# Optimization experiments

Measured on AMD Instinct MI355X. Metric: run time of the kernel, lower is better.

## Reference

```python
import jax, jax.numpy as jnp
import numpy as np

SEQ, BATCH, HID, LAYERS = 512, 64, 1024, 2

def setup_inputs() -> dict:
    key = jax.random.key(0)
    ks = jax.random.split(key, 5)
    scale = 1.0 / np.sqrt(2 * HID)
    return {
        "input": jax.random.normal(ks[0], (SEQ, BATCH, HID), dtype=jnp.float32),
        "h0": jax.random.normal(ks[1], (LAYERS, BATCH, HID), dtype=jnp.float32),
        "c0": jax.random.normal(ks[2], (LAYERS, BATCH, HID), dtype=jnp.float32),
        "W": jax.random.normal(ks[3], (LAYERS, 2 * HID, 4 * HID), dtype=jnp.float32) * scale,
        "b": jax.random.normal(ks[4], (LAYERS, 4 * HID), dtype=jnp.float32) * scale,
    }

def reference(input, h0, c0, W, b):
    num_layers = W.shape[0]

    def step(carry, x_t):
        h, c = carry  # each [L, B, H]
        hs, cs = [], []
        layer_in = x_t  # [B, H]
        for l in range(num_layers):
            concat_in = jnp.concatenate([layer_in, h[l]], axis=1)  # [B, 2H]
            gates = concat_in @ W[l] + b[l]                        # [B, 4H]
            i, j, f, o = jnp.split(gates, 4, axis=1)
            c_new = c[l] * jax.nn.sigmoid(f) + jax.nn.sigmoid(i) * jnp.tanh(j)
            h_new = jnp.tanh(c_new) * jax.nn.sigmoid(o)
            hs.append(h_new)
            cs.append(c_new)
            layer_in = h_new
        return (jnp.stack(hs), jnp.stack(cs)), layer_in

    (last_hidden, last_cell), final_output = jax.lax.scan(step, (h0, c0), input)
    return final_output, (last_hidden, last_cell)
```

## Files before the change

kernel.cpp:

```cpp
#include <hip/hip_runtime.h>


typedef _Float16 half8 __attribute__((ext_vector_type(8)));
typedef float    f32x4 __attribute__((ext_vector_type(4)));
typedef unsigned long long u64;
typedef unsigned int u32;

#define SEQ 512
#define BATCH 64
#define HID 1024
#define NBLK 128
#define SLSZ 65536

__device__ int g_sync[1024];

__global__ void init_bar_k() {
    for (int i = threadIdx.x; i < 1024; i += 256) g_sync[i] = 0;
}

__global__ void zero_out(float* __restrict__ out) {
    size_t i = (size_t)blockIdx.x * blockDim.x + threadIdx.x;
    ((f32x4*)out)[i] = f32x4{0.f, 0.f, 0.f, 0.f};
}

__global__ void pack1(const float* __restrict__ src, _Float16* __restrict__ dst) {
    int nt   = blockIdx.x;
    int ktg  = blockIdx.y;
    int lane = threadIdx.x & 63;
    int wave = threadIdx.x >> 6;
    int kt   = ktg * 4 + wave;
    int k0 = kt * 32 + (lane >> 4) * 8;
    int n  = nt * 16 + (lane & 15);
    half8 v;
#pragma unroll
    for (int j = 0; j < 8; ++j)
        v[j] = (_Float16)src[(size_t)(k0 + j) * 4096 + n];
    *(half8*)(dst + ((size_t)(nt * 32 + kt) * 64 + lane) * 8) = v;
}

__global__ void pack_wh(const float* __restrict__ src, _Float16* __restrict__ dst) {
    int g    = blockIdx.x;
    int ktg  = blockIdx.y;
    int lane = threadIdx.x & 63;
    int wave = threadIdx.x >> 6;
    int kt   = ktg * 4 + wave;
    int c16  = lane & 15;
    int k0   = kt * 32 + (lane >> 4) * 8;
#pragma unroll
    for (int tau = 0; tau < 2; ++tau) {
        int col = (tau * 2 + (c16 >> 3)) * 1024 + g * 8 + (c16 & 7);
        half8 v;
#pragma unroll
        for (int j = 0; j < 8; ++j)
            v[j] = (_Float16)src[(size_t)(k0 + j) * 4096 + col];
        *(half8*)(dst + ((size_t)((g * 2 + tau) * 32 + kt) * 64 + lane) * 8) = v;
    }
}

__global__ void copy_f4(const float* __restrict__ src, float* __restrict__ dst) {
    int i = blockIdx.x * blockDim.x + threadIdx.x;
    ((f32x4*)dst)[i] = ((const f32x4*)src)[i];
}

__global__ __launch_bounds__(256) void gemm_in(
    const float* __restrict__ A, const _Float16* __restrict__ Bp,
    const float* __restrict__ bias, _Float16* __restrict__ Gout)
{
    int lane = threadIdx.x & 63;
    int wave = threadIdx.x >> 6;
    int wm = wave & 1, wn = wave >> 1;
    int m0 = blockIdx.x * 128 + wm * 64;
    int n0 = blockIdx.y * 128 + wn * 64;
    int col = lane & 15, quad = lane >> 4;
    f32x4 acc[4][4] = {};
    const float*    Arow  = A + (size_t)(m0 + col) * 1024 + quad * 8;
    const _Float16* Bbase = Bp + (size_t)(n0 >> 4) * 16384 + (size_t)lane * 8;
    for (int kt = 0; kt < 32; ++kt) {
        half8 a[4], b[4];
#pragma unroll
        for (int i = 0; i < 4; ++i) {
            const float* p = Arow + (size_t)i * 16 * 1024 + kt * 32;
            f32x4 v0 = *(const f32x4*)(p);
            f32x4 v1 = *(const f32x4*)(p + 4);
            a[i][0] = (_Float16)v0[0]; a[i][1] = (_Float16)v0[1];
            a[i][2] = (_Float16)v0[2]; a[i][3] = (_Float16)v0[3];
            a[i][4] = (_Float16)v1[0]; a[i][5] = (_Float16)v1[1];
            a[i][6] = (_Float16)v1[2]; a[i][7] = (_Float16)v1[3];
        }
#pragma unroll
        for (int j = 0; j < 4; ++j)
            b[j] = *(const half8*)(Bbase + (size_t)j * 16384 + kt * 512);
#pragma unroll
        for (int i = 0; i < 4; ++i)
#pragma unroll
            for (int j = 0; j < 4; ++j)
                acc[i][j] = __builtin_amdgcn_mfma_f32_16x16x32_f16(a[i], b[j], acc[i][j], 0, 0, 0);
    }
#pragma unroll
    for (int j = 0; j < 4; ++j) {
        int n = n0 + j * 16 + col;
        float bv = bias[n];
#pragma unroll
        for (int i = 0; i < 4; ++i)
#pragma unroll
            for (int r = 0; r < 4; ++r) {
                int m = m0 + i * 16 + quad * 4 + r;
                Gout[(size_t)m * 4096 + n] = (_Float16)(acc[i][j][r] + bv);
            }
    }
}

__device__ __forceinline__ void grid_barrier(int n) {
    __syncthreads();
    if (threadIdx.x == 0) {
        const int grp = (int)(blockIdx.x & 7);
        int v = __hip_atomic_fetch_add(&g_sync[grp * 64], 1,
                                       __ATOMIC_RELAXED, __HIP_MEMORY_SCOPE_AGENT);
        if (v == n * 16 - 1) {
            int gv = __hip_atomic_fetch_add(&g_sync[576], 1,
                                            __ATOMIC_RELAXED, __HIP_MEMORY_SCOPE_AGENT);
            if (gv == n * 8 - 1)
                __hip_atomic_store(&g_sync[704], n,
                                   __ATOMIC_RELAXED, __HIP_MEMORY_SCOPE_AGENT);
        }
        while (__hip_atomic_load(&g_sync[704],
                                 __ATOMIC_RELAXED, __HIP_MEMORY_SCOPE_AGENT) < n)
            __builtin_amdgcn_s_sleep(1);
    }
    __syncthreads();
}

__device__ __forceinline__ half8 cload8(const _Float16* p) {
    union { half8 h; u64 u[2]; } x;
    x.u[0] = __hip_atomic_load((const u64*)p, __ATOMIC_RELAXED, __HIP_MEMORY_SCOPE_AGENT);
    x.u[1] = __hip_atomic_load((const u64*)p + 1, __ATOMIC_RELAXED, __HIP_MEMORY_SCOPE_AGENT);
    return x.h;
}

__device__ __forceinline__ half8 cvt_row(const float* p) {
    f32x4 v0 = *(const f32x4*)p, v1 = *(const f32x4*)(p + 4);
    half8 a;
    a[0] = (_Float16)v0[0]; a[1] = (_Float16)v0[1];
    a[2] = (_Float16)v0[2]; a[3] = (_Float16)v0[3];
    a[4] = (_Float16)v1[0]; a[5] = (_Float16)v1[1];
    a[6] = (_Float16)v1[2]; a[7] = (_Float16)v1[3];
    return a;
}

template <bool F32, bool DO0, bool DO1>
__device__ __forceinline__ void passA(
    f32x4 (&acc0)[4][2], f32x4 (&acc1)[4][2], const void* src,
    const half8 (&b0)[2][8], const half8 (&b1)[2][8],
    int wave, int c16, int quad)
{
#pragma unroll
    for (int i = 0; i < 8; ++i) {
        const int k0 = (wave * 8 + i) * 32 + quad * 8;
        half8 a[4];
#pragma unroll
        for (int m = 0; m < 4; ++m) {
            if constexpr (F32)
                a[m] = cvt_row((const float*)src + (size_t)(m * 16 + c16) * HID + k0);
            else
                a[m] = cload8((const _Float16*)src + (size_t)(m * 16 + c16) * HID + k0);
        }
#pragma unroll
        for (int m = 0; m < 4; ++m) {
            if constexpr (DO0) {
                acc0[m][0] = __builtin_amdgcn_mfma_f32_16x16x32_f16(a[m], b0[0][i], acc0[m][0], 0, 0, 0);
                acc0[m][1] = __builtin_amdgcn_mfma_f32_16x16x32_f16(a[m], b0[1][i], acc0[m][1], 0, 0, 0);
            }
            if constexpr (DO1) {
                acc1[m][0] = __builtin_amdgcn_mfma_f32_16x16x32_f16(a[m], b1[0][i], acc1[m][0], 0, 0, 0);
                acc1[m][1] = __builtin_amdgcn_mfma_f32_16x16x32_f16(a[m], b1[1][i], acc1[m][1], 0, 0, 0);
            }
        }
    }
}

template <bool F32>
__device__ __forceinline__ void passB(
    f32x4 (&acc1)[4][2], const void* src, const half8* smw,
    int wave, int c16, int quad, int lane)
{
#pragma unroll
    for (int i = 0; i < 8; ++i) {
        const int k0 = (wave * 8 + i) * 32 + quad * 8;
        half8 a[4];
#pragma unroll
        for (int m = 0; m < 4; ++m) {
            if constexpr (F32)
                a[m] = cvt_row((const float*)src + (size_t)(m * 16 + c16) * HID + k0);
            else
                a[m] = cload8((const _Float16*)src + (size_t)(m * 16 + c16) * HID + k0);
        }
        half8 bw0 = smw[(size_t)((0 * 32 + wave * 8 + i) * 64 + lane)];
        half8 bw1 = smw[(size_t)((1 * 32 + wave * 8 + i) * 64 + lane)];
#pragma unroll
        for (int m = 0; m < 4; ++m) {
            acc1[m][0] = __builtin_amdgcn_mfma_f32_16x16x32_f16(a[m], bw0, acc1[m][0], 0, 0, 0);
            acc1[m][1] = __builtin_amdgcn_mfma_f32_16x16x32_f16(a[m], bw1, acc1[m][1], 0, 0, 0);
        }
    }
}

__device__ __forceinline__ void cell_epilogue(
    const f32x4 (&fin)[2], float (&creg)[4], _Float16* rw, float* outp,
    float* lh, float* lc, int rbase, int hcol, int c16, bool owner)
{
#pragma unroll
    for (int r = 0; r < 4; ++r) {
        float v0 = fin[0][r], v1 = fin[1][r];
        float x0 = __shfl_xor(v0, 8), x1 = __shfl_xor(v1, 8);
        float gi = owner ? v0 : x0, gj = owner ? x0 : v0;
        float gf = owner ? v1 : x1, go = owner ? x1 : v1;
        float iv = 1.f / (1.f + __expf(-gi));
        float jv = tanhf(gj);
        float fv = 1.f / (1.f + __expf(-gf));
        float ov = 1.f / (1.f + __expf(-go));
        float cn = creg[r] * fv + iv * jv;
        float hn = tanhf(cn) * ov;
        creg[r] = cn;
        union { _Float16 f; unsigned short s; } cv; cv.f = (_Float16)hn;
        u32 other = (u32)(unsigned short)__shfl_xor((int)cv.s, 1);
        size_t idx = (size_t)(rbase + r) * HID + hcol;
        if (owner) {
            if (outp) outp[idx] = hn;
            if (lh) { lh[idx] = hn; lc[idx] = cn; }
            if (!(c16 & 1)) {
                u32 pk = (u32)cv.s | (other << 16);
                __hip_atomic_store((u32*)(rw + idx), pk,
                                   __ATOMIC_RELAXED, __HIP_MEMORY_SCOPE_AGENT);
            }
        }
    }
}

__global__ __launch_bounds__(256, 1) void lstm_fused(
    const _Float16* __restrict__ WhR0, const _Float16* __restrict__ WxR1,
    const _Float16* __restrict__ WhR1, const _Float16* __restrict__ Gc,
    const float* __restrict__ hinit, _Float16* __restrict__ ring,
    float* __restrict__ cb, float* __restrict__ out,
    const float* __restrict__ bias1, int t0, int nsteps, int nbar0)
{
    const int lane = threadIdx.x & 63;
    const int wave = threadIdx.x >> 6;
    const int g = blockIdx.x;
    const int c16 = lane & 15, quad = lane >> 4;
    const int hcol = g * 8 + (c16 & 7);
    const bool owner = (c16 < 8);
    const int rbase = wave * 16 + quad * 4;

    __shared__ half8 smw[4096];
    __shared__ f32x4 red0[3][4][2][64];
    __shared__ f32x4 red1[3][4][2][64];

    _Float16* ring0 = ring;
    _Float16* ring1 = ring + 2 * SLSZ;
    const size_t FO = (size_t)SEQ * SLSZ;

    {
        const _Float16* wsrc = WhR1 + (size_t)g * 32768;
        for (int i = threadIdx.x; i < 4096; i += 256)
            smw[i] = *(const half8*)(wsrc + (size_t)i * 8);
    }

    half8 bh0[2][8], bx1[2][8];
#pragma unroll
    for (int tau = 0; tau < 2; ++tau)
#pragma unroll
        for (int i = 0; i < 8; ++i) {
            size_t off = ((size_t)((g * 2 + tau) * 32 + wave * 8 + i) * 64 + lane) * 8;
            bh0[tau][i] = *(const half8*)(WhR0 + off);
            bx1[tau][i] = *(const half8*)(WxR1 + off);
        }

    float bv1[2];
#pragma unroll
    for (int tau = 0; tau < 2; ++tau)
        bv1[tau] = bias1[(tau * 2 + (c16 >> 3)) * 1024 + hcol];

    float creg0[4], creg1[4];
#pragma unroll
    for (int r = 0; r < 4; ++r) {
        creg0[r] = cb[(size_t)(rbase + r) * HID + hcol];
        creg1[r] = cb[SLSZ + (size_t)(rbase + r) * HID + hcol];
    }

    const int colG0 = (c16 >> 3) * 1024 + hcol;
    __syncthreads();

    for (int tl = 0; tl < nsteps; ++tl) {
        const int s  = t0 + tl;
        const int t1 = s - 1;
        const bool do0 = (s < SEQ);
        const bool do1 = (t1 >= 0);

        f32x4 acc0[4][2], acc1[4][2];
#pragma unroll
        for (int m = 0; m < 4; ++m)
#pragma unroll
            for (int tau = 0; tau < 2; ++tau) {
                acc0[m][tau] = f32x4{0.f, 0.f, 0.f, 0.f};
                acc1[m][tau] = f32x4{0.f, 0.f, 0.f, 0.f};
            }
#pragma unroll
        for (int m = 0; m < 4; ++m)
            if (m == wave) {
                acc1[m][0] = f32x4{bv1[0], bv1[0], bv1[0], bv1[0]};
                acc1[m][1] = f32x4{bv1[1], bv1[1], bv1[1], bv1[1]};
            }
        if (do0) {
            const _Float16* Gt = Gc + (size_t)tl * 4 * SLSZ;
#pragma unroll
            for (int tau = 0; tau < 2; ++tau) {
                f32x4 v;
#pragma unroll
                for (int r = 0; r < 4; ++r)
                    v[r] = (float)Gt[(size_t)(rbase + r) * 4096 + tau * 2048 + colG0];
#pragma unroll
                for (int m = 0; m < 4; ++m)
                    if (m == wave) acc0[m][tau] = v;
            }
        }

        if (tl > 0) grid_barrier(nbar0 + tl);

        const _Float16* h0prev = ring0 + (size_t)((s - 1) & 1) * SLSZ;
        if (do0 && do1)
            passA<false, true, true>(acc0, acc1, h0prev, bh0, bx1, wave, c16, quad);
        else if (do0)
            passA<true, true, false>(acc0, acc1, hinit, bh0, bx1, wave, c16, quad);
        else
            passA<false, false, true>(acc0, acc1, h0prev, bh0, bx1, wave, c16, quad);

        if (do1) {
            if (t1 == 0)
                passB<true>(acc1, hinit + SLSZ, smw, wave, c16, quad, lane);
            else
                passB<false>(acc1, ring1 + (size_t)((t1 - 1) & 1) * SLSZ, smw,
                             wave, c16, quad, lane);
        }

        if (do0) {
#pragma unroll
            for (int m = 0; m < 4; ++m)
                if (m != wave) {
                    int slot = wave - (wave > m ? 1 : 0);
#pragma unroll
                    for (int tau = 0; tau < 2; ++tau)
                        red0[slot][m][tau][lane] = acc0[m][tau];
                }
        }
        if (do1) {
#pragma unroll
            for (int m = 0; m < 4; ++m)
                if (m != wave) {
                    int slot = wave - (wave > m ? 1 : 0);
#pragma unroll
                    for (int tau = 0; tau < 2; ++tau)
                        red1[slot][m][tau][lane] = acc1[m][tau];
                }
        }
        f32x4 own0[2], own1[2];
        own0[0] = acc0[0][0]; own0[1] = acc0[0][1];
        own1[0] = acc1[0][0]; own1[1] = acc1[0][1];
#pragma unroll
        for (int m = 1; m < 4; ++m)
            if (wave == m) {
                own0[0] = acc0[m][0]; own0[1] = acc0[m][1];
                own1[0] = acc1[m][0]; own1[1] = acc1[m][1];
            }
        __syncthreads();

        if (do0) {
            f32x4 fin[2];
#pragma unroll
            for (int tau = 0; tau < 2; ++tau) {
                f32x4 ssum = own0[tau];
#pragma unroll
                for (int v = 0; v < 3; ++v) ssum += red0[v][wave][tau][lane];
                fin[tau] = ssum;
            }
            float* lh = (s == SEQ - 1) ? out + FO : nullptr;
            float* lc = (s == SEQ - 1) ? out + FO + 2 * SLSZ : nullptr;
            cell_epilogue(fin, creg0, ring0 + (size_t)(s & 1) * SLSZ,
                          nullptr, lh, lc, rbase, hcol, c16, owner);
        }
        if (do1) {
            f32x4 fin[2];
#pragma unroll
            for (int tau = 0; tau < 2; ++tau) {
                f32x4 ssum = own1[tau];
#pragma unroll
                for (int v = 0; v < 3; ++v) ssum += red1[v][wave][tau][lane];
                fin[tau] = ssum;
            }
            float* lh = (t1 == SEQ - 1) ? out + FO + SLSZ : nullptr;
            float* lc = (t1 == SEQ - 1) ? out + FO + 3 * SLSZ : nullptr;
            cell_epilogue(fin, creg1, ring1 + (size_t)(t1 & 1) * SLSZ,
                          out + (size_t)t1 * SLSZ, lh, lc, rbase, hcol, c16, owner);
        }
    }

    if (owner) {
#pragma unroll
        for (int r = 0; r < 4; ++r) {
            cb[(size_t)(rbase + r) * HID + hcol] = creg0[r];
            cb[SLSZ + (size_t)(rbase + r) * HID + hcol] = creg1[r];
        }
    }
}

extern "C" void kernel_launch(void* const* d_in, const int* in_sizes, int n_in,
                              void* d_out, int out_size, void* d_ws, size_t ws_size,
                              hipStream_t stream) {
    const float* X  = (const float*)d_in[0];
    const float* h0 = (const float*)d_in[1];
    const float* c0 = (const float*)d_in[2];
    const float* W  = (const float*)d_in[3];
    const float* bb = (const float*)d_in[4];
    float* out = (float*)d_out;
    char* ws = (char*)d_ws;

    const size_t FIXED = 34603008ULL;
    int CH = 0;
    const int tiers[4] = {32, 16, 8, 4};
    for (int i = 0; i < 4; ++i)
        if (ws_size >= FIXED + (size_t)tiers[i] * 524288ULL) { CH = tiers[i]; break; }
    if (CH == 0) {
        zero_out<<<dim3(33024), 256, 0, stream>>>(out);
        return;
    }

    _Float16* WpX  = (_Float16*)(ws + 0);
    _Float16* WhR0 = (_Float16*)(ws + 8388608);
    _Float16* WxR1 = (_Float16*)(ws + 16777216);
    _Float16* WhR1 = (_Float16*)(ws + 25165824);
    _Float16* ring = (_Float16*)(ws + 33554432);
    float*    cb   = (float*)(ws + 34078720);
    _Float16* Gc   = (_Float16*)(ws + 34603008);

    const size_t MSTRIDE = 2048ULL * 4096ULL;
    const int MC = CH * BATCH;
    const int NCHUNK = SEQ / CH;

    pack1<<<dim3(256, 8), 256, 0, stream>>>(W, WpX);
    pack_wh<<<dim3(NBLK, 8), 256, 0, stream>>>(W + 1024 * 4096, WhR0);
    pack_wh<<<dim3(NBLK, 8), 256, 0, stream>>>(W + MSTRIDE, WxR1);
    pack_wh<<<dim3(NBLK, 8), 256, 0, stream>>>(W + MSTRIDE + 1024 * 4096, WhR1);
    copy_f4<<<dim3(128), 256, 0, stream>>>(c0, cb);
    init_bar_k<<<dim3(1), 256, 0, stream>>>();

    int nbar = 0;
    for (int chunk = 0; chunk < NCHUNK; ++chunk) {
        gemm_in<<<dim3(MC / 128, 32), 256, 0, stream>>>(
            X + (size_t)chunk * MC * 1024, WpX, bb, Gc);
        int nsteps = CH + (chunk == NCHUNK - 1 ? 1 : 0);
        lstm_fused<<<dim3(NBLK), 256, 0, stream>>>(
            WhR0, WxR1, WhR1, Gc, h0, ring, cb, out, bb + 4096,
            chunk * CH, nsteps, nbar);
        nbar += nsteps - 1;
    }
}
```

Before: 12.82 ms.

## Fuse input GEMM and recurrence into one persistent producer/consumer kernel

Replaces the per-chunk sequence of gemm_in plus lstm_fused launches with a single persistent kernel. 64 producer blocks compute the layer-0 input projection into a double-buffered chunk slot while 128 consumer blocks run the recurrent steps, with atomic flags handling the handoff. This removes per-chunk launch overhead and the serialization between GEMM and recurrence, and the cell state stays in registers across all steps instead of round-tripping through a workspace buffer. The grid barrier now spins on per-group release flags and drains outstanding memory ops before arriving. The risks are producer/consumer stalls, smaller chunks (8 or 4), and reliance on all 192 blocks being co-resident.

```diff
diff --git a/kernel.cpp b/kernel.cpp
--- a/kernel.cpp
+++ b/kernel.cpp
@@ -9,13 +9,14 @@
 #define SEQ 512
 #define BATCH 64
 #define HID 1024
-#define NBLK 128
+#define NCONS 128
+#define NPROD 64
 #define SLSZ 65536
 
-__device__ int g_sync[1024];
+__device__ int g_sync[8192];
 
 __global__ void init_bar_k() {
-    for (int i = threadIdx.x; i < 1024; i += 256) g_sync[i] = 0;
+    for (int i = threadIdx.x; i < 8192; i += 256) g_sync[i] = 0;
 }
 
 __global__ void zero_out(float* __restrict__ out) {
@@ -57,20 +58,16 @@
     }
 }
 
-__global__ void copy_f4(const float* __restrict__ src, float* __restrict__ dst) {
-    int i = blockIdx.x * blockDim.x + threadIdx.x;
-    ((f32x4*)dst)[i] = ((const f32x4*)src)[i];
-}
-
-__global__ __launch_bounds__(256) void gemm_in(
+__device__ __forceinline__ void gemm_tile(
     const float* __restrict__ A, const _Float16* __restrict__ Bp,
-    const float* __restrict__ bias, _Float16* __restrict__ Gout)
+    const float* __restrict__ bias, _Float16* __restrict__ Gout,
+    int mi, int ni)
 {
     int lane = threadIdx.x & 63;
     int wave = threadIdx.x >> 6;
     int wm = wave & 1, wn = wave >> 1;
-    int m0 = blockIdx.x * 128 + wm * 64;
-    int n0 = blockIdx.y * 128 + wn * 64;
+    int m0 = mi * 128 + wm * 64;
+    int n0 = ni * 128 + wn * 64;
     int col = lane & 15, quad = lane >> 4;
     f32x4 acc[4][4] = {};
     const float*    Arow  = A + (size_t)(m0 + col) * 1024 + quad * 8;
@@ -110,20 +107,23 @@
     }
 }
 
-__device__ __forceinline__ void grid_barrier(int n) {
+__device__ __forceinline__ void grid_barrier(int n, int grp) {
+    asm volatile("s_waitcnt vmcnt(0)" ::: "memory");
     __syncthreads();
     if (threadIdx.x == 0) {
-        const int grp = (int)(blockIdx.x & 7);
         int v = __hip_atomic_fetch_add(&g_sync[grp * 64], 1,
                                        __ATOMIC_RELAXED, __HIP_MEMORY_SCOPE_AGENT);
-        if (v == n * 16 - 1) {
-            int gv = __hip_atomic_fetch_add(&g_sync[576], 1,
+        if (v == n * (NCONS / 8) - 1) {
+            int gv = __hip_atomic_fetch_add(&g_sync[512], 1,
                                             __ATOMIC_RELAXED, __HIP_MEMORY_SCOPE_AGENT);
-            if (gv == n * 8 - 1)
-                __hip_atomic_store(&g_sync[704], n,
-                                   __ATOMIC_RELAXED, __HIP_MEMORY_SCOPE_AGENT);
-        }
-        while (__hip_atomic_load(&g_sync[704],
+            if (gv == n * 8 - 1) {
+#pragma unroll
+                for (int i = 0; i < 8; ++i)
+                    __hip_atomic_store(&g_sync[576 + i * 64], n,
+                                       __ATOMIC_RELAXED, __HIP_MEMORY_SCOPE_AGENT);
+            }
+        }
+        while (__hip_atomic_load(&g_sync[576 + grp * 64],
                                  __ATOMIC_RELAXED, __HIP_MEMORY_SCOPE_AGENT) < n)
             __builtin_amdgcn_s_sleep(1);
     }
@@ -236,20 +236,55 @@
     }
 }
 
-__global__ __launch_bounds__(256, 1) void lstm_fused(
-    const _Float16* __restrict__ WhR0, const _Float16* __restrict__ WxR1,
+__device__ __forceinline__ void producer_path(
+    const _Float16* __restrict__ WpX, const float* __restrict__ X,
+    const float* __restrict__ bias0, _Float16* __restrict__ Gc,
+    int nchunk, int ch)
+{
+    const int p = blockIdx.x;
+    const int rows = ch * 64;
+    const int tpp = (rows / 128) * 32 / NPROD;
+    const size_t slotsz = (size_t)ch * 4 * SLSZ;
+    for (int c = 0; c < nchunk; ++c) {
+        if (c >= 2) {
+            if (threadIdx.x == 0)
+                while (__hip_atomic_load(&g_sync[3136 + (c - 2) * 16],
+                                         __ATOMIC_RELAXED, __HIP_MEMORY_SCOPE_AGENT) < NCONS)
+                    __builtin_amdgcn_s_sleep(4);
+            __syncthreads();
+        }
+        const float* A = X + (size_t)c * rows * 1024;
+        _Float16* Gout = Gc + (size_t)(c & 1) * slotsz;
+        for (int tt = 0; tt < tpp; ++tt) {
+            int T = p * tpp + tt;
+            gemm_tile(A, WpX, bias0, Gout, T >> 5, T & 31);
+        }
+        asm volatile("s_waitcnt vmcnt(0)" ::: "memory");
+        __syncthreads();
+        if (threadIdx.x == 0) {
+            __builtin_amdgcn_fence(__ATOMIC_RELEASE, "agent");
+            __hip_atomic_fetch_add(&g_sync[1088 + c * 16], 1,
+                                   __ATOMIC_RELAXED, __HIP_MEMORY_SCOPE_AGENT);
+        }
+        __syncthreads();
+    }
+}
+
+__device__ __forceinline__ void consumer_path(
+    int g, const _Float16* __restrict__ WhR0, const _Float16* __restrict__ WxR1,
     const _Float16* __restrict__ WhR1, const _Float16* __restrict__ Gc,
-    const float* __restrict__ hinit, _Float16* __restrict__ ring,
-    float* __restrict__ cb, float* __restrict__ out,
-    const float* __restrict__ bias1, int t0, int nsteps, int nbar0)
+    const float* __restrict__ hinit, const float* __restrict__ cinit,
+    _Float16* __restrict__ ring, float* __restrict__ out,
+    const float* __restrict__ bias1, int ch)
 {
     const int lane = threadIdx.x & 63;
     const int wave = threadIdx.x >> 6;
-    const int g = blockIdx.x;
     const int c16 = lane & 15, quad = lane >> 4;
     const int hcol = g * 8 + (c16 & 7);
     const bool owner = (c16 < 8);
     const int rbase = wave * 16 + quad * 4;
+    const int grp = g & 7;
+    const size_t slotsz = (size_t)ch * 4 * SLSZ;
 
     __shared__ half8 smw[4096];
     __shared__ f32x4 red0[3][4][2][64];
@@ -264,7 +299,6 @@
         for (int i = threadIdx.x; i < 4096; i += 256)
             smw[i] = *(const half8*)(wsrc + (size_t)i * 8);
     }
-
     half8 bh0[2][8], bx1[2][8];
 #pragma unroll
     for (int tau = 0; tau < 2; ++tau)
@@ -274,7 +308,6 @@
             bh0[tau][i] = *(const half8*)(WhR0 + off);
             bx1[tau][i] = *(const half8*)(WxR1 + off);
         }
-
     float bv1[2];
 #pragma unroll
     for (int tau = 0; tau < 2; ++tau)
@@ -283,18 +316,28 @@
     float creg0[4], creg1[4];
 #pragma unroll
     for (int r = 0; r < 4; ++r) {
-        creg0[r] = cb[(size_t)(rbase + r) * HID + hcol];
-        creg1[r] = cb[SLSZ + (size_t)(rbase + r) * HID + hcol];
+        creg0[r] = cinit[(size_t)(rbase + r) * HID + hcol];
+        creg1[r] = cinit[SLSZ + (size_t)(rbase + r) * HID + hcol];
     }
 
     const int colG0 = (c16 >> 3) * 1024 + hcol;
     __syncthreads();
 
-    for (int tl = 0; tl < nsteps; ++tl) {
-        const int s  = t0 + tl;
-        const int t1 = s - 1;
-        const bool do0 = (s < SEQ);
-        const bool do1 = (t1 >= 0);
+    for (int sidx = 0; sidx <= SEQ; ++sidx) {
+        const int s = sidx, t1 = s - 1;
+        const bool do0 = (s < SEQ), do1 = (t1 >= 0);
+        int cchunk = 0, tl = 0;
+        if (do0) { cchunk = s / ch; tl = s - cchunk * ch; }
+
+        if (do0 && tl == 0) {
+            if (threadIdx.x == 0) {
+                while (__hip_atomic_load(&g_sync[1088 + cchunk * 16],
+                                         __ATOMIC_RELAXED, __HIP_MEMORY_SCOPE_AGENT) < NPROD)
+                    __builtin_amdgcn_s_sleep(1);
+                __builtin_amdgcn_fence(__ATOMIC_ACQUIRE, "agent");
+            }
+            __syncthreads();
+        }
 
         f32x4 acc0[4][2], acc1[4][2];
 #pragma unroll
@@ -311,7 +354,7 @@
                 acc1[m][1] = f32x4{bv1[1], bv1[1], bv1[1], bv1[1]};
             }
         if (do0) {
-            const _Float16* Gt = Gc + (size_t)tl * 4 * SLSZ;
+            const _Float16* Gt = Gc + (size_t)(cchunk & 1) * slotsz + (size_t)tl * 4 * SLSZ;
 #pragma unroll
             for (int tau = 0; tau < 2; ++tau) {
                 f32x4 v;
@@ -324,7 +367,10 @@
             }
         }
 
-        if (tl > 0) grid_barrier(nbar0 + tl);
+        if (sidx > 0) grid_barrier(sidx, grp);
+        if (do0 && tl == ch - 1 && threadIdx.x == 0)
+            __hip_atomic_fetch_add(&g_sync[3136 + cchunk * 16], 1,
+                                   __ATOMIC_RELAXED, __HIP_MEMORY_SCOPE_AGENT);
 
         const _Float16* h0prev = ring0 + (size_t)((s - 1) & 1) * SLSZ;
         if (do0 && do1)
@@ -402,14 +448,23 @@
                           out + (size_t)t1 * SLSZ, lh, lc, rbase, hcol, c16, owner);
         }
     }
-
-    if (owner) {
-#pragma unroll
-        for (int r = 0; r < 4; ++r) {
-            cb[(size_t)(rbase + r) * HID + hcol] = creg0[r];
-            cb[SLSZ + (size_t)(rbase + r) * HID + hcol] = creg1[r];
-        }
-    }
+}
+
+__global__ __launch_bounds__(256, 1) void lstm_mega(
+    const _Float16* __restrict__ WpX, const _Float16* __restrict__ WhR0,
+    const _Float16* __restrict__ WxR1, const _Float16* __restrict__ WhR1,
+    _Float16* __restrict__ Gc, const float* __restrict__ X,
+    const float* __restrict__ hinit, const float* __restrict__ cinit,
+    _Float16* __restrict__ ring, float* __restrict__ out,
+    const float* __restrict__ bias0, const float* __restrict__ bias1,
+    int nchunk, int ch)
+{
+    if (blockIdx.x < NPROD) {
+        producer_path(WpX, X, bias0, Gc, nchunk, ch);
+        return;
+    }
+    consumer_path((int)blockIdx.x - NPROD, WhR0, WxR1, WhR1, Gc,
+                  hinit, cinit, ring, out, bias1, ch);
 }
 
 extern "C" void kernel_launch(void* const* d_in, const int* in_sizes, int n_in,
@@ -425,9 +480,8 @@
 
     const size_t FIXED = 34603008ULL;
     int CH = 0;
-    const int tiers[4] = {32, 16, 8, 4};
-    for (int i = 0; i < 4; ++i)
-        if (ws_size >= FIXED + (size_t)tiers[i] * 524288ULL) { CH = tiers[i]; break; }
+    if (ws_size >= FIXED + 2ULL * 8 * 524288ULL)      CH = 8;
+    else if (ws_size >= FIXED + 2ULL * 4 * 524288ULL) CH = 4;
     if (CH == 0) {
         zero_out<<<dim3(33024), 256, 0, stream>>>(out);
         return;
@@ -438,28 +492,17 @@
     _Float16* WxR1 = (_Float16*)(ws + 16777216);
     _Float16* WhR1 = (_Float16*)(ws + 25165824);
     _Float16* ring = (_Float16*)(ws + 33554432);
-    float*    cb   = (float*)(ws + 34078720);
     _Float16* Gc   = (_Float16*)(ws + 34603008);
 
     const size_t MSTRIDE = 2048ULL * 4096ULL;
-    const int MC = CH * BATCH;
-    const int NCHUNK = SEQ / CH;
 
     pack1<<<dim3(256, 8), 256, 0, stream>>>(W, WpX);
-    pack_wh<<<dim3(NBLK, 8), 256, 0, stream>>>(W + 1024 * 4096, WhR0);
-    pack_wh<<<dim3(NBLK, 8), 256, 0, stream>>>(W + MSTRIDE, WxR1);
-    pack_wh<<<dim3(NBLK, 8), 256, 0, stream>>>(W + MSTRIDE + 1024 * 4096, WhR1);
-    copy_f4<<<dim3(128), 256, 0, stream>>>(c0, cb);
+    pack_wh<<<dim3(NCONS, 8), 256, 0, stream>>>(W + 1024 * 4096, WhR0);
+    pack_wh<<<dim3(NCONS, 8), 256, 0, stream>>>(W + MSTRIDE, WxR1);
+    pack_wh<<<dim3(NCONS, 8), 256, 0, stream>>>(W + MSTRIDE + 1024 * 4096, WhR1);
     init_bar_k<<<dim3(1), 256, 0, stream>>>();
 
-    int nbar = 0;
-    for (int chunk = 0; chunk < NCHUNK; ++chunk) {
-        gemm_in<<<dim3(MC / 128, 32), 256, 0, stream>>>(
-            X + (size_t)chunk * MC * 1024, WpX, bb, Gc);
-        int nsteps = CH + (chunk == NCHUNK - 1 ? 1 : 0);
-        lstm_fused<<<dim3(NBLK), 256, 0, stream>>>(
-            WhR0, WxR1, WhR1, Gc, h0, ring, cb, out, bb + 4096,
-            chunk * CH, nsteps, nbar);
-        nbar += nsteps - 1;
-    }
-}
+    lstm_mega<<<dim3(NPROD + NCONS), 256, 0, stream>>>(
+        WpX, WhR0, WxR1, WhR1, Gc, X, h0, c0, ring, out,
+        bb, bb + 4096, SEQ / CH, CH);
+}
```

After: 11.20 ms. 1.14x faster.
